# Kernel tuning notes

Hardware: AMD Instinct MI355X
Metric: run time of the kernel (lower is better)

## Reference

```python
import jax, jax.numpy as jnp
import numpy as np

B, S, F, H, DK = 16, 1024, 512, 8, 64
NEG = 999999.0

def setup_inputs() -> dict:
    key = jax.random.key(0)
    ks = jax.random.split(key, 10)
    s = 1.0 / np.sqrt(F)
    inp = {
        'x': jax.random.normal(ks[0], (B, S, F), dtype=jnp.float32),
        'xlen': jax.random.randint(ks[1], (B,), 1, S + 1, dtype=jnp.int32),
        'WQw': jax.random.uniform(ks[2], (H, DK, F), jnp.float32, -s, s),
        'WQb': jax.random.uniform(ks[3], (H, DK), jnp.float32, -s, s),
        'WKw': jax.random.uniform(ks[4], (H, DK, F), jnp.float32, -s, s),
        'WKb': jax.random.uniform(ks[5], (H, DK), jnp.float32, -s, s),
        'WVw': jax.random.uniform(ks[6], (H, DK, F), jnp.float32, -s, s),
        'WVb': jax.random.uniform(ks[7], (H, DK), jnp.float32, -s, s),
        'WOw': jax.random.uniform(ks[8], (F, H * DK), jnp.float32, -1.0/np.sqrt(H*DK), 1.0/np.sqrt(H*DK)),
        'WOb': jax.random.uniform(ks[9], (F,), jnp.float32, -1.0/np.sqrt(H*DK), 1.0/np.sqrt(H*DK)),
    }
    return inp

def reference(x, xlen, WQw, WQb, WKw, WKb, WVw, WVb, WOw, WOb):
    # batched per-head projections: [B,S,F] x [H,DK,F] -> [B,H,S,DK]
    q = jnp.einsum('bsf,hdf->bhsd', x, WQw) + WQb[None, :, None, :]
    k = jnp.einsum('bsf,hdf->bhsd', x, WKw) + WKb[None, :, None, :]
    v = jnp.einsum('bsf,hdf->bhsd', x, WVw) + WVb[None, :, None, :]
    scores = jnp.einsum('bhsd,bhtd->bhst', q, k) / jnp.sqrt(jnp.float32(DK))
    # additive padding mask; original masks key positions >= xlen[j]-1 (off-by-one preserved)
    key_pos = jnp.arange(S)[None, :]                       # [1,S]
    mask = jnp.where(key_pos >= (xlen - 1)[:, None], -NEG, 0.0).astype(jnp.float32)
    scores = scores + mask[:, None, None, :]               # [B,H,S,S]
    attn = jax.nn.softmax(scores, axis=-1)
    z = jnp.einsum('bhst,bhtd->bhsd', attn, v)             # [B,H,S,DK]
    z = jnp.transpose(z, (0, 2, 1, 3)).reshape(B, S, H * DK)  # concat heads
    return z @ WOw.T + WOb
```

## Files before the change

### kernel.cpp

```cpp
#include <hip/hip_runtime.h>
#include <hip/hip_bf16.h>

typedef short bf16x8 __attribute__((ext_vector_type(8)));
typedef float f32x4 __attribute__((ext_vector_type(4)));
typedef unsigned short u16;

#define B_   16
#define S_   1024
#define F_   512
#define H_   8
#define DK_  64


__device__ __forceinline__ u16 f2bf(float f) {
    union { float f; unsigned int u; } v; v.f = f;
    return (u16)((v.u + 0x7FFFu + ((v.u >> 16) & 1u)) >> 16);
}
__device__ __forceinline__ float bf2f(u16 h) {
    union { unsigned int u; float f; } v; v.u = ((unsigned int)h) << 16;
    return v.f;
}
__device__ __forceinline__ bf16x8 cvt8(float4 a, float4 b) {
    union { u16 u[8]; bf16x8 v; } r;
    r.u[0] = f2bf(a.x); r.u[1] = f2bf(a.y); r.u[2] = f2bf(a.z); r.u[3] = f2bf(a.w);
    r.u[4] = f2bf(b.x); r.u[5] = f2bf(b.y); r.u[6] = f2bf(b.z); r.u[7] = f2bf(b.w);
    return r.v;
}
__device__ __forceinline__ unsigned int pk2(float lo, float hi) {
    union { __hip_bfloat162 h; unsigned int u; } c;
    c.h = __float22bfloat162_rn(make_float2(lo, hi));
    return c.u;
}

__device__ __forceinline__ void gl_lds16(const u16* g, u16* l) {
    __builtin_amdgcn_global_load_lds(
        (const __attribute__((address_space(1))) unsigned int*)g,
        (__attribute__((address_space(3))) unsigned int*)l,
        16, 0, 0);
}

__global__ __launch_bounds__(256) void cvt_all(
    const float* __restrict__ x,
    const float* __restrict__ wq, const float* __restrict__ wk,
    const float* __restrict__ wv, const float* __restrict__ wo,
    const float* __restrict__ bq, const float* __restrict__ bk,
    const float* __restrict__ bv, const float* __restrict__ bo,
    u16* __restrict__ Xbf, u16* __restrict__ Wbase)
{
    const size_t u = (size_t)blockIdx.x * 256 + threadIdx.x;
    const float* src; u16* dst;
    if (u < 1048576)      { src = x  + u * 8;               dst = Xbf + u * 8; }
    else if (u < 1081344) { src = wq + (u - 1048576) * 8;   dst = Wbase + (u - 1048576) * 8; }
    else if (u < 1114112) { src = wk + (u - 1081344) * 8;   dst = Wbase +  262144 + (u - 1081344) * 8; }
    else if (u < 1146880) { src = wv + (u - 1114112) * 8;   dst = Wbase +  524288 + (u - 1114112) * 8; }
    else if (u < 1179648) { src = wo + (u - 1146880) * 8;   dst = Wbase +  786432 + (u - 1146880) * 8; }
    else if (u < 1179712) { src = bq + (u - 1179648) * 8;   dst = Wbase + 1048576 + (u - 1179648) * 8; }
    else if (u < 1179776) { src = bk + (u - 1179712) * 8;   dst = Wbase + 1049088 + (u - 1179712) * 8; }
    else if (u < 1179840) { src = bv + (u - 1179776) * 8;   dst = Wbase + 1049600 + (u - 1179776) * 8; }
    else                  { src = bo + (u - 1179840) * 8;   dst = Wbase + 1050112 + (u - 1179840) * 8; }
    *(bf16x8*)dst = cvt8(*(const float4*)src, *(const float4*)(src + 4));
}

template <int EPI>
__global__ __launch_bounds__(256) void gemm128(
    const u16* __restrict__ A, const u16* __restrict__ Bm,
    const u16* __restrict__ bias, void* __restrict__ out)
{
    __shared__ __align__(16) u16 AsL[4096];
    __shared__ __align__(16) u16 BsL[4096];

    const int t    = threadIdx.x;
    const int wave = t >> 6, lane = t & 63;
    const int l15  = lane & 15, quad = lane >> 4;
    const int wr   = (wave & 1) * 64, wc = (wave >> 1) * 64;
    const int m0   = blockIdx.x * 128, n0 = blockIdx.y * 128;
    const int sr   = t >> 2, scol = (t & 3) * 8;

    f32x4 acc[4][4];
#pragma unroll
    for (int i = 0; i < 4; i++)
#pragma unroll
        for (int j = 0; j < 4; j++) acc[i][j] = {0.f, 0.f, 0.f, 0.f};

    const u16* Ab = A  + (size_t)(m0 + sr) * 512 + scol;
    const u16* Bb = Bm + (size_t)(n0 + sr) * 512 + scol;
    u16* la = &AsL[t * 8];
    u16* lb = &BsL[t * 8];

    for (int k0 = 0; k0 < 512; k0 += 32) {
        gl_lds16(Ab + k0,         la);
        gl_lds16(Ab + 32768 + k0, la + 2048);
        gl_lds16(Bb + k0,         lb);
        gl_lds16(Bb + 32768 + k0, lb + 2048);
        __syncthreads();
        bf16x8 af[4], bfv[4];
#pragma unroll
        for (int i = 0; i < 4; i++) af[i]  = *(const bf16x8*)&AsL[(wr + i * 16 + l15) * 32 + quad * 8];
#pragma unroll
        for (int j = 0; j < 4; j++) bfv[j] = *(const bf16x8*)&BsL[(wc + j * 16 + l15) * 32 + quad * 8];
#pragma unroll
        for (int i = 0; i < 4; i++)
#pragma unroll
            for (int j = 0; j < 4; j++)
                acc[i][j] = __builtin_amdgcn_mfma_f32_16x16x32_bf16(af[i], bfv[j], acc[i][j], 0, 0, 0);
        __syncthreads();
    }

#pragma unroll
    for (int j = 0; j < 4; j++) {
        const int n  = n0 + wc + j * 16 + l15;
        const float bv = bf2f(bias[n]);
        const int hh = n >> 6, d = n & 63;
#pragma unroll
        for (int i = 0; i < 4; i++) {
#pragma unroll
            for (int r = 0; r < 4; r++) {
                const int m = m0 + wr + i * 16 + quad * 4 + r;
                const float val = acc[i][j][r] + bv;
                if (EPI == 0) {
                    const int b = m >> 10, s = m & 1023;
                    ((u16*)out)[((size_t)(b * 8 + hh) * 1024 + s) * 64 + d] = f2bf(val);
                } else if (EPI == 1) {
                    const int b = m >> 10, s = m & 1023;
                    ((u16*)out)[((size_t)(b * 8 + hh) * 64 + d) * 1024 + s] = f2bf(val);
                } else {
                    ((float*)out)[(size_t)m * 512 + n] = val;
                }
            }
        }
    }
}

__global__ __launch_bounds__(256) void attn(
    const u16* __restrict__ Xbf, const u16* __restrict__ Wqbf,
    const u16* __restrict__ bqbf,
    const u16* __restrict__ Kg, const u16* __restrict__ Vt,
    const int* __restrict__ xlen, u16* __restrict__ Z)
{
    __shared__ __align__(16) u16 smem[13824];

    const int t    = threadIdx.x;
    const int wave = t >> 6, lane = t & 63;
    const int l15  = lane & 15, quad = lane >> 4;
    const int bh   = blockIdx.y, b = bh >> 3, h = bh & 7;
    const int bx   = blockIdx.x;
    const int xm1  = xlen[b] - 1;
    const int wm   = (wave & 1) * 32, wn = (wave >> 1) * 32;

    u16* Ks = smem;
    u16* Vs = smem + 4608;
    u16* Qs = smem + 9216;

    f32x4 qa[2][2];
#pragma unroll
    for (int i = 0; i < 2; i++)
#pragma unroll
        for (int j = 0; j < 2; j++) qa[i][j] = {0.f, 0.f, 0.f, 0.f};

    const int sr = t >> 2, scol = (t & 3) * 8;
    const u16* Xb = Xbf  + (size_t)(b * 1024 + bx * 64 + sr) * 512 + scol;
    const u16* Wb = Wqbf + (size_t)(h * 64 + sr) * 512 + scol;
    u16* la = &smem[t * 8];
    u16* lb = &smem[2048 + t * 8];

    for (int k0 = 0; k0 < 512; k0 += 32) {
        gl_lds16(Xb + k0, la);
        gl_lds16(Wb + k0, lb);
        __syncthreads();
        bf16x8 af[2], bfv[2];
#pragma unroll
        for (int i = 0; i < 2; i++) af[i]  = *(const bf16x8*)&smem[(wm + i * 16 + l15) * 32 + quad * 8];
#pragma unroll
        for (int j = 0; j < 2; j++) bfv[j] = *(const bf16x8*)&smem[2048 + (wn + j * 16 + l15) * 32 + quad * 8];
#pragma unroll
        for (int i = 0; i < 2; i++)
#pragma unroll
            for (int j = 0; j < 2; j++)
                qa[i][j] = __builtin_amdgcn_mfma_f32_16x16x32_bf16(af[i], bfv[j], qa[i][j], 0, 0, 0);
        __syncthreads();
    }
#pragma unroll
    for (int j = 0; j < 2; j++) {
        const int d  = wn + j * 16 + l15;
        const float bv = bf2f(bqbf[h * 64 + d]);
#pragma unroll
        for (int i = 0; i < 2; i++) {
#pragma unroll
            for (int r = 0; r < 4; r++) {
                const int row = wm + i * 16 + quad * 4 + r;
                Qs[row * 72 + d] = f2bf((qa[i][j][r] + bv) * 0.125f);
            }
        }
    }
    __syncthreads();

    bf16x8 aq[2];
#pragma unroll
    for (int kk = 0; kk < 2; kk++)
        aq[kk] = *(const bf16x8*)&Qs[(wave * 16 + l15) * 72 + kk * 32 + quad * 8];

    const size_t baseKV = (size_t)bh * (S_ * DK_);
    const bool domask = (xm1 >= 1);
    const int  Slim   = domask ? xm1 : S_;

    f32x4 o[4];
#pragma unroll
    for (int j = 0; j < 4; j++) o[j] = {0.f, 0.f, 0.f, 0.f};
    float li = 0.f;

    const int srow = t >> 3, scl = (t & 7) * 8;
    const int prow = ((srow >> 2) & 1) * 16 + (srow >> 3) * 4 + (srow & 3);

    for (int t0 = 0; t0 < Slim; t0 += 64) {
        *(uint4*)&Ks[prow * 72 + scl]        = *(const uint4*)&Kg[baseKV + (size_t)(t0 + srow) * 64 + scl];
        *(uint4*)&Ks[(prow + 32) * 72 + scl] = *(const uint4*)&Kg[baseKV + (size_t)(t0 + srow + 32) * 64 + scl];
        *(uint4*)&Vs[srow * 72 + scl]        = *(const uint4*)&Vt[baseKV + (size_t)srow * 1024 + t0 + scl];
        *(uint4*)&Vs[(srow + 32) * 72 + scl] = *(const uint4*)&Vt[baseKV + (size_t)(srow + 32) * 1024 + t0 + scl];
        __syncthreads();

        f32x4 sc[4];
#pragma unroll
        for (int nh = 0; nh < 4; nh++) {
            f32x4 s = {0.f, 0.f, 0.f, 0.f};
#pragma unroll
            for (int kk = 0; kk < 2; kk++) {
                bf16x8 bk = *(const bf16x8*)&Ks[(nh * 16 + l15) * 72 + kk * 32 + quad * 8];
                s = __builtin_amdgcn_mfma_f32_16x16x32_bf16(bk, aq[kk], s, 0, 0, 0);
            }
            sc[nh] = s;
        }
        if (domask && (t0 + 64 > xm1)) {
#pragma unroll
            for (int nh = 0; nh < 4; nh++) {
                const int kb = t0 + ((nh >> 1) << 5) + (quad << 3) + ((nh & 1) << 2);
#pragma unroll
                for (int r = 0; r < 4; r++)
                    sc[nh][r] += ((kb + r) >= xm1) ? -999999.0f : 0.0f;
            }
        }
#pragma unroll
        for (int nh = 0; nh < 4; nh++) {
#pragma unroll
            for (int r = 0; r < 4; r++) sc[nh][r] = __expf(sc[nh][r]);
            li += (sc[nh][0] + sc[nh][1]) + (sc[nh][2] + sc[nh][3]);
        }
        union { unsigned int u[4]; bf16x8 v; } ap0, ap1;
        ap0.u[0] = pk2(sc[0][0], sc[0][1]); ap0.u[1] = pk2(sc[0][2], sc[0][3]);
        ap0.u[2] = pk2(sc[1][0], sc[1][1]); ap0.u[3] = pk2(sc[1][2], sc[1][3]);
        ap1.u[0] = pk2(sc[2][0], sc[2][1]); ap1.u[1] = pk2(sc[2][2], sc[2][3]);
        ap1.u[2] = pk2(sc[3][0], sc[3][1]); ap1.u[3] = pk2(sc[3][2], sc[3][3]);
#pragma unroll
        for (int j = 0; j < 4; j++) {
            bf16x8 bv0 = *(const bf16x8*)&Vs[(j * 16 + l15) * 72 + quad * 8];
            o[j] = __builtin_amdgcn_mfma_f32_16x16x32_bf16(ap0.v, bv0, o[j], 0, 0, 0);
            bf16x8 bv1 = *(const bf16x8*)&Vs[(j * 16 + l15) * 72 + 32 + quad * 8];
            o[j] = __builtin_amdgcn_mfma_f32_16x16x32_bf16(ap1.v, bv1, o[j], 0, 0, 0);
        }
        __syncthreads();
    }

    float rs = li;
    rs += __shfl_xor(rs, 16);
    rs += __shfl_xor(rs, 32);
    const float linv = 1.0f / rs;
    float lr[4];
#pragma unroll
    for (int r = 0; r < 4; r++) lr[r] = __shfl(linv, quad * 4 + r);

#pragma unroll
    for (int j = 0; j < 4; j++) {
#pragma unroll
        for (int r = 0; r < 4; r++) {
            const int s = bx * 64 + wave * 16 + quad * 4 + r;
            Z[((size_t)(b * 1024 + s)) * 512 + h * 64 + j * 16 + l15] = f2bf(o[j][r] * lr[r]);
        }
    }
}

extern "C" void kernel_launch(void* const* d_in, const int* in_sizes, int n_in,
                              void* d_out, int out_size, void* d_ws, size_t ws_size,
                              hipStream_t stream)
{
    (void)in_sizes; (void)n_in; (void)out_size; (void)ws_size;

    const float* x    = (const float*)d_in[0];
    const int*   xlen = (const int*)d_in[1];
    const float* WQw  = (const float*)d_in[2];
    const float* WQb  = (const float*)d_in[3];
    const float* WKw  = (const float*)d_in[4];
    const float* WKb  = (const float*)d_in[5];
    const float* WVw  = (const float*)d_in[6];
    const float* WVb  = (const float*)d_in[7];
    const float* WOw  = (const float*)d_in[8];
    const float* WOb  = (const float*)d_in[9];

    const size_t NQ = (size_t)B_ * H_ * S_ * DK_;
    u16* Kb    = (u16*)d_ws;
    u16* Zb    = Kb + NQ;
    u16* Wbase = Zb + NQ;
    u16* WQbf  = Wbase;
    u16* WKbf  = Wbase + 262144;
    u16* WVbf  = Wbase + 524288;
    u16* WObf  = Wbase + 786432;
    u16* bqbf  = Wbase + 1048576;
    u16* bkbf  = Wbase + 1049088;
    u16* bvbf  = Wbase + 1049600;
    u16* bobf  = Wbase + 1050112;
    u16* Xbf = (u16*)d_out;
    u16* Vb  = Xbf + NQ;

    dim3 blk(256);
    cvt_all<<<dim3(4609), blk, 0, stream>>>(x, WQw, WKw, WVw, WOw,
                                            WQb, WKb, WVb, WOb, Xbf, Wbase);

    dim3 gGemm(128, 4);
    gemm128<0><<<gGemm, blk, 0, stream>>>(Xbf, WKbf, bkbf, Kb);
    gemm128<1><<<gGemm, blk, 0, stream>>>(Xbf, WVbf, bvbf, Vb);

    dim3 gAttn(16, 128);
    attn<<<gAttn, blk, 0, stream>>>(Xbf, WQbf, bqbf, Kb, Vb, xlen, Zb);

    gemm128<2><<<gGemm, blk, 0, stream>>>(Zb, WObf, bobf, d_out);
}
```

Baseline: 204.5 us.

## Double-buffer LDS tiles in GEMM and fused Q-projection loops

Turns the single-buffered K loops in the 128x128 GEMM and in the attention kernel's Q projection into two-stage pipelines. The tile for step k+2 is loaded from global memory into LDS while step k is computed, with explicit vmcnt waits and barriers. This is meant to hide global-load latency that was previously exposed at each syncthreads. It doubles LDS use per block, which may lower occupancy, and the attention kernel's smem layout must fit the 4096-offset B buffer before Qs at 9216. Bias loads are also hoisted ahead of the main loop.

```diff
diff --git a/kernel.cpp b/kernel.cpp
--- a/kernel.cpp
+++ b/kernel.cpp
@@ -66,8 +66,8 @@
     const u16* __restrict__ A, const u16* __restrict__ Bm,
     const u16* __restrict__ bias, void* __restrict__ out)
 {
-    __shared__ __align__(16) u16 AsL[4096];
-    __shared__ __align__(16) u16 BsL[4096];
+    __shared__ __align__(16) u16 AsL[2][4096];
+    __shared__ __align__(16) u16 BsL[2][4096];
 
     const int t    = threadIdx.x;
     const int wave = t >> 6, lane = t & 63;
@@ -76,6 +76,10 @@
     const int m0   = blockIdx.x * 128, n0 = blockIdx.y * 128;
     const int sr   = t >> 2, scol = (t & 3) * 8;
 
+    float bvp[4];
+#pragma unroll
+    for (int j = 0; j < 4; j++) bvp[j] = bf2f(bias[n0 + wc + j * 16 + l15]);
+
     f32x4 acc[4][4];
 #pragma unroll
     for (int i = 0; i < 4; i++)
@@ -84,32 +88,61 @@
 
     const u16* Ab = A  + (size_t)(m0 + sr) * 512 + scol;
     const u16* Bb = Bm + (size_t)(n0 + sr) * 512 + scol;
-    u16* la = &AsL[t * 8];
-    u16* lb = &BsL[t * 8];
-
-    for (int k0 = 0; k0 < 512; k0 += 32) {
-        gl_lds16(Ab + k0,         la);
-        gl_lds16(Ab + 32768 + k0, la + 2048);
-        gl_lds16(Bb + k0,         lb);
-        gl_lds16(Bb + 32768 + k0, lb + 2048);
-        __syncthreads();
+
+    gl_lds16(Ab,              &AsL[0][t * 8]);
+    gl_lds16(Ab + 32768,      &AsL[0][2048 + t * 8]);
+    gl_lds16(Bb,              &BsL[0][t * 8]);
+    gl_lds16(Bb + 32768,      &BsL[0][2048 + t * 8]);
+    gl_lds16(Ab + 32,         &AsL[1][t * 8]);
+    gl_lds16(Ab + 32768 + 32, &AsL[1][2048 + t * 8]);
+    gl_lds16(Bb + 32,         &BsL[1][t * 8]);
+    gl_lds16(Bb + 32768 + 32, &BsL[1][2048 + t * 8]);
+
+    for (int t0 = 0; t0 < 15; ++t0) {
+        asm volatile("s_waitcnt vmcnt(4)" ::: "memory");
+        __builtin_amdgcn_s_barrier();
+        __builtin_amdgcn_sched_barrier(0);
+        const int c = t0 & 1;
         bf16x8 af[4], bfv[4];
 #pragma unroll
-        for (int i = 0; i < 4; i++) af[i]  = *(const bf16x8*)&AsL[(wr + i * 16 + l15) * 32 + quad * 8];
-#pragma unroll
-        for (int j = 0; j < 4; j++) bfv[j] = *(const bf16x8*)&BsL[(wc + j * 16 + l15) * 32 + quad * 8];
+        for (int i = 0; i < 4; i++) af[i]  = *(const bf16x8*)&AsL[c][(wr + i * 16 + l15) * 32 + quad * 8];
+#pragma unroll
+        for (int j = 0; j < 4; j++) bfv[j] = *(const bf16x8*)&BsL[c][(wc + j * 16 + l15) * 32 + quad * 8];
 #pragma unroll
         for (int i = 0; i < 4; i++)
 #pragma unroll
             for (int j = 0; j < 4; j++)
                 acc[i][j] = __builtin_amdgcn_mfma_f32_16x16x32_bf16(af[i], bfv[j], acc[i][j], 0, 0, 0);
-        __syncthreads();
+        __builtin_amdgcn_sched_barrier(0);
+        __builtin_amdgcn_s_barrier();
+        if (t0 < 14) {
+            const int k0n = (t0 + 2) * 32;
+            gl_lds16(Ab + k0n,         &AsL[c][t * 8]);
+            gl_lds16(Ab + 32768 + k0n, &AsL[c][2048 + t * 8]);
+            gl_lds16(Bb + k0n,         &BsL[c][t * 8]);
+            gl_lds16(Bb + 32768 + k0n, &BsL[c][2048 + t * 8]);
+        }
+    }
+    asm volatile("s_waitcnt vmcnt(0)" ::: "memory");
+    __builtin_amdgcn_s_barrier();
+    __builtin_amdgcn_sched_barrier(0);
+    {
+        bf16x8 af[4], bfv[4];
+#pragma unroll
+        for (int i = 0; i < 4; i++) af[i]  = *(const bf16x8*)&AsL[1][(wr + i * 16 + l15) * 32 + quad * 8];
+#pragma unroll
+        for (int j = 0; j < 4; j++) bfv[j] = *(const bf16x8*)&BsL[1][(wc + j * 16 + l15) * 32 + quad * 8];
+#pragma unroll
+        for (int i = 0; i < 4; i++)
+#pragma unroll
+            for (int j = 0; j < 4; j++)
+                acc[i][j] = __builtin_amdgcn_mfma_f32_16x16x32_bf16(af[i], bfv[j], acc[i][j], 0, 0, 0);
     }
 
 #pragma unroll
     for (int j = 0; j < 4; j++) {
         const int n  = n0 + wc + j * 16 + l15;
-        const float bv = bf2f(bias[n]);
+        const float bv = bvp[j];
         const int hh = n >> 6, d = n & 63;
 #pragma unroll
         for (int i = 0; i < 4; i++) {
@@ -160,29 +193,58 @@
     const int sr = t >> 2, scol = (t & 3) * 8;
     const u16* Xb = Xbf  + (size_t)(b * 1024 + bx * 64 + sr) * 512 + scol;
     const u16* Wb = Wqbf + (size_t)(h * 64 + sr) * 512 + scol;
-    u16* la = &smem[t * 8];
-    u16* lb = &smem[2048 + t * 8];
-
-    for (int k0 = 0; k0 < 512; k0 += 32) {
-        gl_lds16(Xb + k0, la);
-        gl_lds16(Wb + k0, lb);
-        __syncthreads();
+
+    float bqp[2];
+#pragma unroll
+    for (int j = 0; j < 2; j++) bqp[j] = bf2f(bqbf[h * 64 + wn + j * 16 + l15]);
+
+    gl_lds16(Xb,      &smem[t * 8]);
+    gl_lds16(Wb,      &smem[4096 + t * 8]);
+    gl_lds16(Xb + 32, &smem[2048 + t * 8]);
+    gl_lds16(Wb + 32, &smem[4096 + 2048 + t * 8]);
+
+    for (int it = 0; it < 15; ++it) {
+        asm volatile("s_waitcnt vmcnt(2)" ::: "memory");
+        __builtin_amdgcn_s_barrier();
+        __builtin_amdgcn_sched_barrier(0);
+        const int c = it & 1;
         bf16x8 af[2], bfv[2];
 #pragma unroll
-        for (int i = 0; i < 2; i++) af[i]  = *(const bf16x8*)&smem[(wm + i * 16 + l15) * 32 + quad * 8];
-#pragma unroll
-        for (int j = 0; j < 2; j++) bfv[j] = *(const bf16x8*)&smem[2048 + (wn + j * 16 + l15) * 32 + quad * 8];
+        for (int i = 0; i < 2; i++) af[i]  = *(const bf16x8*)&smem[c * 2048 + (wm + i * 16 + l15) * 32 + quad * 8];
+#pragma unroll
+        for (int j = 0; j < 2; j++) bfv[j] = *(const bf16x8*)&smem[4096 + c * 2048 + (wn + j * 16 + l15) * 32 + quad * 8];
 #pragma unroll
         for (int i = 0; i < 2; i++)
 #pragma unroll
             for (int j = 0; j < 2; j++)
                 qa[i][j] = __builtin_amdgcn_mfma_f32_16x16x32_bf16(af[i], bfv[j], qa[i][j], 0, 0, 0);
-        __syncthreads();
+        __builtin_amdgcn_sched_barrier(0);
+        __builtin_amdgcn_s_barrier();
+        if (it < 14) {
+            const int k0n = (it + 2) * 32;
+            gl_lds16(Xb + k0n, &smem[c * 2048 + t * 8]);
+            gl_lds16(Wb + k0n, &smem[4096 + c * 2048 + t * 8]);
+        }
+    }
+    asm volatile("s_waitcnt vmcnt(0)" ::: "memory");
+    __builtin_amdgcn_s_barrier();
+    __builtin_amdgcn_sched_barrier(0);
+    {
+        bf16x8 af[2], bfv[2];
+#pragma unroll
+        for (int i = 0; i < 2; i++) af[i]  = *(const bf16x8*)&smem[2048 + (wm + i * 16 + l15) * 32 + quad * 8];
+#pragma unroll
+        for (int j = 0; j < 2; j++) bfv[j] = *(const bf16x8*)&smem[4096 + 2048 + (wn + j * 16 + l15) * 32 + quad * 8];
+#pragma unroll
+        for (int i = 0; i < 2; i++)
+#pragma unroll
+            for (int j = 0; j < 2; j++)
+                qa[i][j] = __builtin_amdgcn_mfma_f32_16x16x32_bf16(af[i], bfv[j], qa[i][j], 0, 0, 0);
     }
 #pragma unroll
     for (int j = 0; j < 2; j++) {
         const int d  = wn + j * 16 + l15;
-        const float bv = bf2f(bqbf[h * 64 + d]);
+        const float bv = bqp[j];
 #pragma unroll
         for (int i = 0; i < 2; i++) {
 #pragma unroll
```

After: 200.4 us. -2.0%, faster.
